# Optimization experiments

Hardware: AMD Instinct MI355X
Metric: run time of the kernel (lower is better)

Reference implementation:

```python
import jax, jax.numpy as jnp
import numpy as np

B, NB, H, E, NCT, NL = 16, 4096, 128, 65536, 32, 2
LN_EPS = 1e-5


def _layernorm(x, scale, bias):
    mu = jnp.mean(x, axis=-1, keepdims=True)
    var = jnp.var(x, axis=-1, keepdims=True)
    return (x - mu) / jnp.sqrt(var + LN_EPS) * scale + bias


def setup_inputs() -> dict:
    key = jax.random.key(0)
    ks = jax.random.split(key, 18)
    s = 1.0 / np.sqrt(H)
    inp = {
        'block_tokens': jax.random.normal(ks[0], (B, NB, H), jnp.float32),
        'edge_structure': jnp.full((E,), 0.5, jnp.float32),
        'ct_emb': 0.1 * jax.random.normal(ks[1], (NCT, E), jnp.float32),
        'W_proj': s * jax.random.normal(ks[2], (H, H), jnp.float32),
        'b_proj': jnp.zeros((H,), jnp.float32),
        'W_gate': (1.0 / np.sqrt(2 * H)) * jax.random.normal(ks[3], (2 * H, H), jnp.float32),
        'b_gate': jnp.zeros((H,), jnp.float32),
        'ln_scale': jnp.ones((NL, H), jnp.float32),
        'ln_bias': jnp.zeros((NL, H), jnp.float32),
        'W1': s * jax.random.normal(ks[4], (NL, H, 2 * H), jnp.float32),
        'b1': jnp.zeros((NL, 2 * H), jnp.float32),
        'W2': (1.0 / np.sqrt(2 * H)) * jax.random.normal(ks[5], (NL, 2 * H, H), jnp.float32),
        'b2': jnp.zeros((NL, H), jnp.float32),
        'cancer_type': jax.random.randint(ks[6], (B,), 0, NCT),
        'edge_src': jax.random.randint(ks[7], (E,), 0, NB),
        'edge_dst': jax.random.randint(ks[8], (E,), 0, NB),
        'block_active': jax.random.bernoulli(ks[9], 0.9, (B, NB)),
    }
    return inp


def reference(block_tokens, edge_structure, ct_emb, W_proj, b_proj, W_gate, b_gate,
              ln_scale, ln_bias, W1, b1, W2, b2,
              cancer_type, edge_src, edge_dst, block_active):
    # per-edge signed weights, masked by active src/dst blocks  -> (B, E)
    structure = jax.nn.sigmoid(edge_structure)
    edge_w = structure[None, :] * ct_emb[cancer_type]
    edge_w = edge_w * block_active[:, edge_src].astype(edge_w.dtype) \
                    * block_active[:, edge_dst].astype(edge_w.dtype)
    # route projection + ELU
    h_route = jax.nn.elu(jnp.einsum('bnh,hd->bnd', block_tokens, W_proj) + b_proj)
    # gather sources, weight, scatter-add to destinations
    weighted = edge_w[..., None] * h_route[:, edge_src, :]          # (B, E, H)
    messages = jnp.zeros_like(block_tokens).at[:, edge_dst, :].add(weighted)
    # gated residual
    gate = jax.nn.sigmoid(
        jnp.einsum('bnh,hd->bnd', jnp.concatenate([block_tokens, messages], axis=-1), W_gate) + b_gate)
    x = block_tokens + gate * messages
    # norm + FFN layers (dropout is identity at inference)
    for l in range(NL):
        normed = _layernorm(x, ln_scale[l], ln_bias[l])
        h = jax.nn.elu(jnp.einsum('bnh,hf->bnf', normed, W1[l]) + b1[l])
        x = x + jnp.einsum('bnf,fh->bnh', h, W2[l]) + b2[l]
    return (x, edge_w)
```

## Files before the change

kernel.cpp:

```cpp
#include <hip/hip_runtime.h>
#include <hip/hip_bf16.h>

#define BB     16
#define NBLK   4096
#define HD     128
#define NE     65536
#define MTOT   (BB * NBLK)

typedef __attribute__((ext_vector_type(8))) short bf16x8;
typedef __attribute__((ext_vector_type(4))) float f32x4;

__device__ __forceinline__ float bf2f(unsigned short u) {
    union { unsigned int i; float f; } v; v.i = ((unsigned int)u) << 16; return v.f;
}
__device__ __forceinline__ unsigned short f2bf(float f) {
    union { float f; unsigned int i; } v; v.f = f;
    unsigned int u = v.i;
    unsigned int r = u + 0x7FFFu + ((u >> 16) & 1u);
    return (unsigned short)(r >> 16);
}
__device__ __forceinline__ float ldf(const void* p, size_t i, int f32m) {
    return f32m ? ((const float*)p)[i] : bf2f(((const unsigned short*)p)[i]);
}
__device__ __forceinline__ int get_active(const void* p, int i, int mode) {
    switch (mode) {
        case 1:  return ((const unsigned char*)p)[i] != 0;
        case 2:  return ((const unsigned short*)p)[i] != 0;
        case 3:  return ((const float*)p)[i] != 0.f;
        default: return ((const int*)p)[i] != 0;
    }
}
__device__ __forceinline__ float elu_f(float v) {
    const float e = __expf(v);
    return v > 0.f ? v : e - 1.f;
}
__device__ __forceinline__ float sig_f(float v) {
    return 1.f / (1.f + __expf(-v));
}

__global__ void probe_k(const unsigned int* __restrict__ es,
                        const unsigned int* __restrict__ act,
                        int* __restrict__ flags)
{
    const int lane = threadIdx.x;
    const unsigned int v0 = act[lane], v1 = act[64 + lane];
    auto le1  = [](unsigned int v) { return v <= 1u; };
    auto byt  = [](unsigned int v) {
        return ((v & 0xFFu) <= 1u) && (((v >> 8) & 0xFFu) <= 1u) &&
               (((v >> 16) & 0xFFu) <= 1u) && ((v >> 24) <= 1u); };
    auto f32b = [](unsigned int v) { return v == 0u || v == 0x3F800000u; };
    auto bfb  = [](unsigned int v) {
        unsigned short h0 = (unsigned short)(v & 0xFFFFu), h1 = (unsigned short)(v >> 16);
        return (h0 == 0u || h0 == 0x3F80u) && (h1 == 0u || h1 == 0x3F80u); };
    const unsigned long long m_le1 = __ballot(le1(v0) && le1(v1));
    const unsigned long long m_byt = __ballot(byt(v0) && byt(v1));
    const unsigned long long m_f32 = __ballot(f32b(v0) && f32b(v1));
    const unsigned long long m_bf  = __ballot(bfb(v0) && bfb(v1));
    if (lane == 0) {
        flags[0] = (es[0] != 0x3F003F00u) ? 1 : 0;
        const unsigned long long full = ~0ull;
        flags[1] = (m_le1 == full) ? 0
                 : (m_byt == full) ? 1
                 : (m_f32 == full) ? 3
                 : (m_bf  == full) ? 2 : 0;
    }
}

__global__ __launch_bounds__(256) void cvt_k(const void* __restrict__ bt,
                                             unsigned short* __restrict__ bt16,
                                             const int* __restrict__ flags)
{
    const size_t i = ((size_t)blockIdx.x * 256 + threadIdx.x) * 8;
    if (flags[0]) {
        const float* q = (const float*)bt + i;
        f32x4 lo = *(const f32x4*)q;
        f32x4 hi = *(const f32x4*)(q + 4);
        bf16x8 r;
        #pragma unroll
        for (int j = 0; j < 4; ++j) { r[j] = (short)f2bf(lo[j]); r[4 + j] = (short)f2bf(hi[j]); }
        *(bf16x8*)(bt16 + i) = r;
    } else {
        *(bf16x8*)(bt16 + i) = *(const bf16x8*)((const unsigned short*)bt + i);
    }
}

__global__ __launch_bounds__(256) void transpose_k(
    const void* p0, const void* p1, const void* p2, const void* p3,
    const void* p4, const void* p5, unsigned short* __restrict__ wsT,
    const int* __restrict__ flags)
{
    const void* srcs[6]  = {p0, p1, p2, p3, p4, p5};
    const int eoffs[6]   = {0, 0, 0, 32768, 0, 32768};
    const int Ks[6]      = {128, 256, 128, 128, 256, 256};
    const int nsh[6]     = {7,   7,   8,   8,   7,   7};
    const int offs[6]    = {0, 16384, 49152, 81920, 114688, 147456};
    const int f32m = flags[0];
    const int z = blockIdx.y;
    const int K = Ks[z];
    const int Nn = 1 << nsh[z];
    const int idx = blockIdx.x * 256 + threadIdx.x;
    if (idx >= K * Nn) return;
    const int k = idx >> nsh[z];
    const int n = idx & (Nn - 1);
    wsT[offs[z] + n * K + k] = f2bf(ldf(srcs[z], (size_t)eoffs[z] + idx, f32m));
}

__global__ __launch_bounds__(256) void csr_count_k(const int* __restrict__ edst,
                                                   int* __restrict__ cnt)
{
    const int e = blockIdx.x * 256 + threadIdx.x;
    atomicAdd(&cnt[edst[e]], 1);
}

__global__ __launch_bounds__(1024) void csr_scan_k(const int* __restrict__ cnt,
                                                   int* __restrict__ ofs,
                                                   int* __restrict__ cur)
{
    __shared__ int part[1024];
    const int t = threadIdx.x;
    const int4 c = ((const int4*)cnt)[t];
    part[t] = c.x + c.y + c.z + c.w;
    __syncthreads();
    #pragma unroll
    for (int off = 1; off < 1024; off <<= 1) {
        const int v = (t >= off) ? part[t - off] : 0;
        __syncthreads();
        part[t] += v;
        __syncthreads();
    }
    const int base = t ? part[t - 1] : 0;
    int4 o;
    o.x = base; o.y = o.x + c.x; o.z = o.y + c.y; o.w = o.z + c.z;
    ((int4*)ofs)[t] = o;
    ((int4*)cur)[t] = o;
    if (t == 1023) ofs[4096] = part[1023];
}

__global__ __launch_bounds__(256) void csr_fill_k(const int* __restrict__ edst,
                                                  int* __restrict__ cur,
                                                  int* __restrict__ eidx,
                                                  int* __restrict__ pos_e)
{
    const int e = blockIdx.x * 256 + threadIdx.x;
    const int pos = atomicAdd(&cur[edst[e]], 1);
    eidx[pos] = e;
    pos_e[e] = pos;
}

__global__ __launch_bounds__(256) void edge_k(
    const void* __restrict__ es, const void* __restrict__ ctE,
    const int* __restrict__ ctype, const int* __restrict__ esrc, const int* __restrict__ edst,
    const void* __restrict__ act, const int* __restrict__ pos_e,
    float* __restrict__ out_ew, float2* __restrict__ compact,
    const int* __restrict__ flags)
{
    const int f32m = flags[0], am = flags[1];
    const int idx = blockIdx.x * 256 + threadIdx.x;
    const int b = idx >> 16;
    const int e = idx & 65535;
    const int s = esrc[e];
    const float sv  = sig_f(ldf(es, e, f32m));
    const float emb = ldf(ctE, (size_t)ctype[b] * NE + e, f32m);
    const int a1 = get_active(act, b * NBLK + s, am);
    const int a2 = get_active(act, b * NBLK + edst[e], am);
    const float w = (a1 && a2) ? sv * emb : 0.f;
    out_ew[idx] = w;
    compact[((size_t)b << 16) + pos_e[e]] = make_float2(w, __int_as_float(s));
}

__global__ __launch_bounds__(256) void gather_k(
    const float2* __restrict__ compact, const int* __restrict__ ofs,
    const unsigned short* __restrict__ hr, unsigned short* __restrict__ msg)
{
    const int blk = blockIdx.x;
    const int xcd = blk & 7;
    const int i   = blk >> 3;
    const int b   = xcd * 2 + (i & 1);
    const int d   = ((i >> 1) << 2) | (threadIdx.x >> 6);
    const int lane = threadIdx.x & 63;
    const int sub  = lane >> 4;
    const int l15  = lane & 15;
    const int j1 = ofs[d + 1];
    const size_t bbase = (size_t)b * NBLK * HD;
    const float2* cb = compact + ((size_t)b << 16);
    float acc[8];
    #pragma unroll
    for (int i2 = 0; i2 < 8; ++i2) acc[i2] = 0.f;
    int j = ofs[d] + sub;
    float2 c = (j < j1) ? cb[j] : make_float2(0.f, 0.f);
    while (j < j1) {
        const int jn = j + 4;
        const float2 cn = (jn < j1) ? cb[jn] : make_float2(0.f, 0.f);
        if (c.x != 0.f) {
            const int src = __float_as_int(c.y);
            const bf16x8 v = *(const bf16x8*)(hr + bbase + (size_t)src * HD + l15 * 8);
            #pragma unroll
            for (int i2 = 0; i2 < 8; ++i2)
                acc[i2] += c.x * bf2f((unsigned short)v[i2]);
        }
        c = cn; j = jn;
    }
    #pragma unroll
    for (int i2 = 0; i2 < 8; ++i2) {
        acc[i2] += __shfl_xor(acc[i2], 16);
        acc[i2] += __shfl_xor(acc[i2], 32);
    }
    if (sub == 0) {
        bf16x8 o;
        #pragma unroll
        for (int i2 = 0; i2 < 8; ++i2) o[i2] = (short)f2bf(acc[i2]);
        *(bf16x8*)(msg + bbase + (size_t)d * HD + l15 * 8) = o;
    }
}

template<int K, int N, int EPI>
__global__ __launch_bounds__(256) void gemm_k(
    const unsigned short* __restrict__ A,
    const unsigned short* __restrict__ WT,
    const void* __restrict__ bias, long boff,
    unsigned short* __restrict__ outb,
    const int* __restrict__ flags)
{
    constexpr int KI    = K / 32;
    constexpr int NCW   = N / 4;
    constexpr int NTW   = NCW / 16;
    constexpr int TILES = 8;
    constexpr int NBUF  = (K == 128 ? 4 : 2);
    const int f32m = flags[0];
    const int t    = threadIdx.x;
    const int lane = t & 63;
    const int wave = t >> 6;
    const int q    = lane >> 4;
    const int l15  = lane & 15;
    const int n0   = wave * NCW;

    bf16x8 Bf[KI][NTW];
    #pragma unroll
    for (int ki = 0; ki < KI; ++ki)
        #pragma unroll
        for (int nt = 0; nt < NTW; ++nt)
            Bf[ki][nt] = *(const bf16x8*)(WT + (size_t)(n0 + nt * 16 + l15) * K + ki * 32 + q * 8);

    float biasv[NTW];
    #pragma unroll
    for (int nt = 0; nt < NTW; ++nt)
        biasv[nt] = ldf(bias, boff + n0 + nt * 16 + l15, f32m);

    const int tile0 = blockIdx.x * TILES;
    bf16x8 Af[NBUF][KI];
    auto loadA = [&](int tt) {
        const int arow = (tile0 + tt) * 16 + l15;
        #pragma unroll
        for (int ki = 0; ki < KI; ++ki)
            Af[tt % NBUF][ki] = *(const bf16x8*)(A + (size_t)arow * K + ki * 32 + q * 8);
    };
    #pragma unroll
    for (int p = 0; p < NBUF; ++p) loadA(p);

    #pragma unroll
    for (int tt = 0; tt < TILES; ++tt) {
        const int s = tt % NBUF;
        f32x4 acc[NTW];
        #pragma unroll
        for (int i = 0; i < NTW; ++i) acc[i] = (f32x4){0.f, 0.f, 0.f, 0.f};
        #pragma unroll
        for (int ki = 0; ki < KI; ++ki)
            #pragma unroll
            for (int nt = 0; nt < NTW; ++nt)
                acc[nt] = __builtin_amdgcn_mfma_f32_16x16x32_bf16(Af[s][ki], Bf[ki][nt], acc[nt], 0, 0, 0);

        if (tt + NBUF < TILES) loadA(tt + NBUF);

        const int m0 = (tile0 + tt) * 16;
        #pragma unroll
        for (int nt = 0; nt < NTW; ++nt) {
            #pragma unroll
            for (int r = 0; r < 4; ++r) {
                const int row = m0 + q * 4 + r;
                const int col = n0 + nt * 16 + l15;
                const float v = acc[nt][r] + biasv[nt];
                outb[(size_t)row * N + col] = f2bf(elu_f(v));
            }
        }
    }
}

#define XI(tl, row, col)  x_lds[tl][row][((col) + 4 * (row)) & 127]
#define UIx(row, col)     U[row][((col) + 8 * (row)) & 255]

__global__ __launch_bounds__(256) void mega_k(
    const unsigned short* __restrict__ bt16,
    const unsigned short* __restrict__ msg,
    const void* __restrict__ btf,
    const unsigned short* __restrict__ WT,
    const void* __restrict__ bg,
    const void* __restrict__ b1, const void* __restrict__ b2,
    const void* __restrict__ lns, const void* __restrict__ lnb,
    float* __restrict__ xout,
    const int* __restrict__ flags)
{
    __shared__ __align__(16) float          x_lds[2][32][128];
    __shared__ __align__(16) unsigned short U[32][256];

    const int f32m = flags[0];
    const int t    = threadIdx.x;
    const int lane = t & 63;
    const int wave = t >> 6;
    const int q    = lane >> 4;
    const int l15  = lane & 15;
    const int base = blockIdx.x * 64;

    const int ng = wave * 32;
    const unsigned short* WgT = WT + 16384;

    bf16x8 Bg[8][2];
    #pragma unroll
    for (int ki = 0; ki < 8; ++ki)
        #pragma unroll
        for (int nt = 0; nt < 2; ++nt)
            Bg[ki][nt] = *(const bf16x8*)(WgT + (size_t)(ng + nt * 16 + l15) * 256 + ki * 32 + q * 8);
    float biasg[2];
    #pragma unroll
    for (int nt = 0; nt < 2; ++nt) biasg[nt] = ldf(bg, ng + nt * 16 + l15, f32m);

    #pragma unroll
    for (int tl = 0; tl < 2; ++tl) {
        const int row0 = base + tl * 32;
        bf16x8 Ag[2][8];
        #pragma unroll
        for (int tt = 0; tt < 2; ++tt) {
            const int arow = row0 + tt * 16 + l15;
            #pragma unroll
            for (int ki = 0; ki < 8; ++ki) {
                const int k = ki * 32 + q * 8;
                Ag[tt][ki] = (k < HD)
                    ? *(const bf16x8*)(bt16 + (size_t)arow * HD + k)
                    : *(const bf16x8*)(msg  + (size_t)arow * HD + (k - HD));
            }
        }
        float btv[2][2][4], mgv[2][2][4];
        #pragma unroll
        for (int tt = 0; tt < 2; ++tt)
            #pragma unroll
            for (int nt = 0; nt < 2; ++nt)
                #pragma unroll
                for (int r = 0; r < 4; ++r) {
                    const size_t gi = (size_t)(row0 + tt * 16 + q * 4 + r) * HD + ng + nt * 16 + l15;
                    btv[tt][nt][r] = ldf(btf, gi, f32m);
                    mgv[tt][nt][r] = bf2f(msg[gi]);
                }
        #pragma unroll
        for (int tt = 0; tt < 2; ++tt) {
            f32x4 acc[2];
            #pragma unroll
            for (int nt = 0; nt < 2; ++nt) acc[nt] = (f32x4){0.f, 0.f, 0.f, 0.f};
            __builtin_amdgcn_s_setprio(1);
            #pragma unroll
            for (int ki = 0; ki < 8; ++ki)
                #pragma unroll
                for (int nt = 0; nt < 2; ++nt)
                    acc[nt] = __builtin_amdgcn_mfma_f32_16x16x32_bf16(Ag[tt][ki], Bg[ki][nt], acc[nt], 0, 0, 0);
            __builtin_amdgcn_s_setprio(0);
            #pragma unroll
            for (int nt = 0; nt < 2; ++nt)
                #pragma unroll
                for (int r = 0; r < 4; ++r) {
                    const float g = sig_f(acc[nt][r] + biasg[nt]);
                    XI(tl, tt * 16 + q * 4 + r, ng + nt * 16 + l15) =
                        btv[tt][nt][r] + g * mgv[tt][nt][r];
                }
        }
    }
    __syncthreads();

    const int rowln = t >> 3;
    const int seg   = t & 7;
    const int n1 = wave * 64;
    const int n2 = wave * 32;

    #pragma unroll
    for (int l = 0; l < 2; ++l) {
        const unsigned short* W1T = WT + (l ? 81920  : 49152);
        const unsigned short* W2T = WT + (l ? 147456 : 114688);
        const long b1o = l ? 256 : 0, b2o = l ? 128 : 0, lno = l ? 128 : 0;

        bf16x8 B1[4][4];
        #pragma unroll
        for (int ki = 0; ki < 4; ++ki)
            #pragma unroll
            for (int nt = 0; nt < 4; ++nt)
                B1[ki][nt] = *(const bf16x8*)(W1T + (size_t)(n1 + nt * 16 + l15) * 128 + ki * 32 + q * 8);
        float bias1[4];
        #pragma unroll
        for (int nt = 0; nt < 4; ++nt) bias1[nt] = ldf(b1, b1o + n1 + nt * 16 + l15, f32m);
        bf16x8 B2[8][2];
        #pragma unroll
        for (int ki = 0; ki < 8; ++ki)
            #pragma unroll
            for (int nt = 0; nt < 2; ++nt)
                B2[ki][nt] = *(const bf16x8*)(W2T + (size_t)(n2 + nt * 16 + l15) * 256 + ki * 32 + q * 8);
        float bias2[2];
        #pragma unroll
        for (int nt = 0; nt < 2; ++nt) bias2[nt] = ldf(b2, b2o + n2 + nt * 16 + l15, f32m);

        float lsv[16], lbv[16];
        #pragma unroll
        for (int j = 0; j < 4; ++j)
            #pragma unroll
            for (int k = 0; k < 4; ++k) {
                const int col = seg * 16 + j * 4 + k;
                lsv[j * 4 + k] = ldf(lns, lno + col, f32m);
                lbv[j * 4 + k] = ldf(lnb, lno + col, f32m);
            }

        #pragma unroll
        for (int tl = 0; tl < 2; ++tl) {
            f32x4 xv[4];
            #pragma unroll
            for (int j = 0; j < 4; ++j)
                xv[j] = *(const f32x4*)&XI(tl, rowln, seg * 16 + j * 4);
            float s = 0.f, ss = 0.f;
            #pragma unroll
            for (int j = 0; j < 4; ++j)
                #pragma unroll
                for (int k = 0; k < 4; ++k) { const float v = xv[j][k]; s += v; ss += v * v; }
            #pragma unroll
            for (int off = 1; off < 8; off <<= 1) { s += __shfl_xor(s, off); ss += __shfl_xor(ss, off); }
            const float mu = s * (1.f / 128.f);
            const float rs = rsqrtf(ss * (1.f / 128.f) - mu * mu + 1e-5f);
            bf16x8 nv[2];
            #pragma unroll
            for (int j = 0; j < 4; ++j)
                #pragma unroll
                for (int k = 0; k < 4; ++k) {
                    const float nn = (xv[j][k] - mu) * rs * lsv[j * 4 + k] + lbv[j * 4 + k];
                    nv[j >> 1][(j & 1) * 4 + k] = (short)f2bf(nn);
                }
            *(bf16x8*)&UIx(rowln, seg * 16)     = nv[0];
            *(bf16x8*)&UIx(rowln, seg * 16 + 8) = nv[1];
            __syncthreads();

            bf16x8 An[2][4];
            #pragma unroll
            for (int tt = 0; tt < 2; ++tt)
                #pragma unroll
                for (int ki = 0; ki < 4; ++ki)
                    An[tt][ki] = *(const bf16x8*)&UIx(tt * 16 + l15, ki * 32 + q * 8);
            __syncthreads();

            #pragma unroll
            for (int tt = 0; tt < 2; ++tt) {
                f32x4 acc[4];
                #pragma unroll
                for (int nt = 0; nt < 4; ++nt) acc[nt] = (f32x4){0.f, 0.f, 0.f, 0.f};
                __builtin_amdgcn_s_setprio(1);
                #pragma unroll
                for (int ki = 0; ki < 4; ++ki)
                    #pragma unroll
                    for (int nt = 0; nt < 4; ++nt)
                        acc[nt] = __builtin_amdgcn_mfma_f32_16x16x32_bf16(An[tt][ki], B1[ki][nt], acc[nt], 0, 0, 0);
                __builtin_amdgcn_s_setprio(0);
                #pragma unroll
                for (int nt = 0; nt < 4; ++nt)
                    #pragma unroll
                    for (int r = 0; r < 4; ++r)
                        UIx(tt * 16 + q * 4 + r, n1 + nt * 16 + l15) =
                            f2bf(elu_f(acc[nt][r] + bias1[nt]));
            }
            __syncthreads();

            #pragma unroll
            for (int tt = 0; tt < 2; ++tt) {
                bf16x8 Ah[8];
                #pragma unroll
                for (int ki = 0; ki < 8; ++ki)
                    Ah[ki] = *(const bf16x8*)&UIx(tt * 16 + l15, ki * 32 + q * 8);
                f32x4 acc[2];
                #pragma unroll
                for (int nt = 0; nt < 2; ++nt) acc[nt] = (f32x4){0.f, 0.f, 0.f, 0.f};
                __builtin_amdgcn_s_setprio(1);
                #pragma unroll
                for (int ki = 0; ki < 8; ++ki)
                    #pragma unroll
                    for (int nt = 0; nt < 2; ++nt)
                        acc[nt] = __builtin_amdgcn_mfma_f32_16x16x32_bf16(Ah[ki], B2[ki][nt], acc[nt], 0, 0, 0);
                __builtin_amdgcn_s_setprio(0);
                #pragma unroll
                for (int nt = 0; nt < 2; ++nt)
                    #pragma unroll
                    for (int r = 0; r < 4; ++r)
                        XI(tl, tt * 16 + q * 4 + r, n2 + nt * 16 + l15) += acc[nt][r] + bias2[nt];
            }
            __syncthreads();
        }
    }

    #pragma unroll
    for (int tl = 0; tl < 2; ++tl) {
        float* xo = xout + (size_t)(base + tl * 32) * HD;
        #pragma unroll
        for (int j = 0; j < 4; ++j) {
            const int idx = j * 256 + t;
            const int r2  = idx >> 5;
            const int c4  = (idx & 31) * 4;
            *(f32x4*)(xo + (size_t)idx * 4) = *(const f32x4*)&XI(tl, r2, c4);
        }
    }
}

extern "C" void kernel_launch(void* const* d_in, const int* in_sizes, int n_in,
                              void* d_out, int out_size, void* d_ws, size_t ws_size,
                              hipStream_t stream)
{
    (void)in_sizes; (void)n_in; (void)out_size; (void)ws_size;

    const void* bt  = d_in[0];
    const void* es  = d_in[1];
    const void* ctE = d_in[2];
    const void* Wp  = d_in[3];
    const void* bp  = d_in[4];
    const void* Wg  = d_in[5];
    const void* bg  = d_in[6];
    const void* lns = d_in[7];
    const void* lnb = d_in[8];
    const void* W1  = d_in[9];
    const void* b1  = d_in[10];
    const void* W2  = d_in[11];
    const void* b2  = d_in[12];
    const int* ctype = (const int*)d_in[13];
    const int* esrc  = (const int*)d_in[14];
    const int* edst  = (const int*)d_in[15];
    const void* act  = d_in[16];

    float* out_x  = (float*)d_out;
    float* out_ew = out_x + (size_t)MTOT * HD;
    float* x = out_x;

    char* ws = (char*)d_ws;
    int*            flags = (int*)ws;
    unsigned short* msg   = (unsigned short*)(ws + 1024);
    unsigned short* bt16  = (unsigned short*)(ws + 1024 + (16ull << 20));
    unsigned short* hr    = (unsigned short*)(ws + 1024 + (32ull << 20));
    char* base48 = ws + 1024 + (48ull << 20);
    int*            cnt     = (int*)(base48);
    int*            ofs     = (int*)(base48 + (16 << 10));
    int*            cur     = (int*)(base48 + (36 << 10));
    int*            eidx    = (int*)(base48 + (52 << 10));
    int*            pos_e   = (int*)(base48 + (308 << 10));
    unsigned short* WT      = (unsigned short*)(base48 + (576 << 10));
    float2*         compact = (float2*)(base48 + (1 << 20));

    const int M = MTOT;

    probe_k<<<1, 64, 0, stream>>>((const unsigned int*)es, (const unsigned int*)act, flags);
    hipMemsetAsync(cnt, 0, NBLK * sizeof(int), stream);

    cvt_k<<<dim3((M * HD / 8) / 256), 256, 0, stream>>>(bt, bt16, flags);
    transpose_k<<<dim3(128, 6), 256, 0, stream>>>(Wp, Wg, W1, W1, W2, W2, WT, flags);

    csr_count_k<<<dim3(NE / 256), 256, 0, stream>>>(edst, cnt);
    csr_scan_k<<<dim3(1), 1024, 0, stream>>>(cnt, ofs, cur);
    csr_fill_k<<<dim3(NE / 256), 256, 0, stream>>>(edst, cur, eidx, pos_e);

    edge_k<<<dim3((BB * NE) / 256), 256, 0, stream>>>(
        es, ctE, ctype, esrc, edst, act, pos_e, out_ew, compact, flags);

    gemm_k<128, 128, 0><<<dim3(M / 128), 256, 0, stream>>>(
        bt16, WT + 0, bp, 0, hr, flags);

    gather_k<<<dim3(M / 4), 256, 0, stream>>>(compact, ofs, hr, msg);

    mega_k<<<dim3(M / 64), 256, 0, stream>>>(
        bt16, msg, bt, WT, bg, b1, b2, lns, lnb, x, flags);
}
```

Baseline: 315.8 us.

## Double mega_k block to 512 threads, batch tiles per barrier, cut register pressure

The fused gate/LN/FFN kernel now runs 512 threads per block, with two halves of four waves each handling 64 rows, so each block covers 128 rows and the grid is halved. Syncthreads are batched across both 32-row tiles per layer, which cuts the number of barriers. W2 fragments are loaded later and the layernorm scale/bias are read inline instead of held in registers, which lowers register pressure so the 512,2 launch bound can fit. LDS use roughly doubles, and the larger barriers involve more waves, so occupancy and stall behaviour shift.

```diff
diff --git a/kernel.cpp b/kernel.cpp
--- a/kernel.cpp
+++ b/kernel.cpp
@@ -285,10 +285,10 @@
     }
 }
 
-#define XI(tl, row, col)  x_lds[tl][row][((col) + 4 * (row)) & 127]
-#define UIx(row, col)     U[row][((col) + 8 * (row)) & 255]
-
-__global__ __launch_bounds__(256) void mega_k(
+#define XI(xt, row, col)      x_lds[xt][row][((col) + 4 * (row)) & 127]
+#define UI(hf, tl, row, col)  U[hf][tl][row][((col) + 8 * (row)) & 255]
+
+__global__ __launch_bounds__(512, 2) void mega_k(
     const unsigned short* __restrict__ bt16,
     const unsigned short* __restrict__ msg,
     const void* __restrict__ btf,
@@ -299,18 +299,20 @@
     float* __restrict__ xout,
     const int* __restrict__ flags)
 {
-    __shared__ __align__(16) float          x_lds[2][32][128];
-    __shared__ __align__(16) unsigned short U[32][256];
+    __shared__ __align__(16) float          x_lds[4][32][128];
+    __shared__ __align__(16) unsigned short U[2][2][32][256];
 
     const int f32m = flags[0];
     const int t    = threadIdx.x;
     const int lane = t & 63;
     const int wave = t >> 6;
+    const int hf   = wave >> 2;
+    const int wv   = wave & 3;
     const int q    = lane >> 4;
     const int l15  = lane & 15;
-    const int base = blockIdx.x * 64;
-
-    const int ng = wave * 32;
+    const int rhf  = blockIdx.x * 128 + hf * 64;
+
+    const int ng = wv * 32;
     const unsigned short* WgT = WT + 16384;
 
     bf16x8 Bg[8][2];
@@ -325,32 +327,27 @@
 
     #pragma unroll
     for (int tl = 0; tl < 2; ++tl) {
-        const int row0 = base + tl * 32;
-        bf16x8 Ag[2][8];
+        const int xt = hf * 2 + tl;
         #pragma unroll
         for (int tt = 0; tt < 2; ++tt) {
-            const int arow = row0 + tt * 16 + l15;
+            const int arow = rhf + tl * 32 + tt * 16;
+            bf16x8 Ag[8];
             #pragma unroll
             for (int ki = 0; ki < 8; ++ki) {
                 const int k = ki * 32 + q * 8;
-                Ag[tt][ki] = (k < HD)
-                    ? *(const bf16x8*)(bt16 + (size_t)arow * HD + k)
-                    : *(const bf16x8*)(msg  + (size_t)arow * HD + (k - HD));
+                Ag[ki] = (k < HD)
+                    ? *(const bf16x8*)(bt16 + (size_t)(arow + l15) * HD + k)
+                    : *(const bf16x8*)(msg  + (size_t)(arow + l15) * HD + (k - HD));
             }
-        }
-        float btv[2][2][4], mgv[2][2][4];
-        #pragma unroll
-        for (int tt = 0; tt < 2; ++tt)
+            float btv[2][4], mgv[2][4];
             #pragma unroll
             for (int nt = 0; nt < 2; ++nt)
                 #pragma unroll
                 for (int r = 0; r < 4; ++r) {
-                    const size_t gi = (size_t)(row0 + tt * 16 + q * 4 + r) * HD + ng + nt * 16 + l15;
-                    btv[tt][nt][r] = ldf(btf, gi, f32m);
-                    mgv[tt][nt][r] = bf2f(msg[gi]);
+                    const size_t gi = (size_t)(arow + q * 4 + r) * HD + ng + nt * 16 + l15;
+                    btv[nt][r] = ldf(btf, gi, f32m);
+                    mgv[nt][r] = bf2f(msg[gi]);
                 }
-        #pragma unroll
-        for (int tt = 0; tt < 2; ++tt) {
             f32x4 acc[2];
             #pragma unroll
             for (int nt = 0; nt < 2; ++nt) acc[nt] = (f32x4){0.f, 0.f, 0.f, 0.f};
@@ -359,24 +356,24 @@
             for (int ki = 0; ki < 8; ++ki)
                 #pragma unroll
                 for (int nt = 0; nt < 2; ++nt)
-                    acc[nt] = __builtin_amdgcn_mfma_f32_16x16x32_bf16(Ag[tt][ki], Bg[ki][nt], acc[nt], 0, 0, 0);
+                    acc[nt] = __builtin_amdgcn_mfma_f32_16x16x32_bf16(Ag[ki], Bg[ki][nt], acc[nt], 0, 0, 0);
             __builtin_amdgcn_s_setprio(0);
             #pragma unroll
             for (int nt = 0; nt < 2; ++nt)
                 #pragma unroll
                 for (int r = 0; r < 4; ++r) {
                     const float g = sig_f(acc[nt][r] + biasg[nt]);
-                    XI(tl, tt * 16 + q * 4 + r, ng + nt * 16 + l15) =
-                        btv[tt][nt][r] + g * mgv[tt][nt][r];
+                    XI(xt, tt * 16 + q * 4 + r, ng + nt * 16 + l15) =
+                        btv[nt][r] + g * mgv[nt][r];
                 }
         }
     }
     __syncthreads();
 
-    const int rowln = t >> 3;
+    const int rowln = (t & 255) >> 3;
     const int seg   = t & 7;
-    const int n1 = wave * 64;
-    const int n2 = wave * 32;
+    const int n1 = wv * 64;
+    const int n2 = wv * 32;
 
     #pragma unroll
     for (int l = 0; l < 2; ++l) {
@@ -393,32 +390,14 @@
         float bias1[4];
         #pragma unroll
         for (int nt = 0; nt < 4; ++nt) bias1[nt] = ldf(b1, b1o + n1 + nt * 16 + l15, f32m);
-        bf16x8 B2[8][2];
-        #pragma unroll
-        for (int ki = 0; ki < 8; ++ki)
-            #pragma unroll
-            for (int nt = 0; nt < 2; ++nt)
-                B2[ki][nt] = *(const bf16x8*)(W2T + (size_t)(n2 + nt * 16 + l15) * 256 + ki * 32 + q * 8);
-        float bias2[2];
-        #pragma unroll
-        for (int nt = 0; nt < 2; ++nt) bias2[nt] = ldf(b2, b2o + n2 + nt * 16 + l15, f32m);
-
-        float lsv[16], lbv[16];
-        #pragma unroll
-        for (int j = 0; j < 4; ++j)
-            #pragma unroll
-            for (int k = 0; k < 4; ++k) {
-                const int col = seg * 16 + j * 4 + k;
-                lsv[j * 4 + k] = ldf(lns, lno + col, f32m);
-                lbv[j * 4 + k] = ldf(lnb, lno + col, f32m);
-            }
 
         #pragma unroll
         for (int tl = 0; tl < 2; ++tl) {
+            const int xt = hf * 2 + tl;
             f32x4 xv[4];
             #pragma unroll
             for (int j = 0; j < 4; ++j)
-                xv[j] = *(const f32x4*)&XI(tl, rowln, seg * 16 + j * 4);
+                xv[j] = *(const f32x4*)&XI(xt, rowln, seg * 16 + j * 4);
             float s = 0.f, ss = 0.f;
             #pragma unroll
             for (int j = 0; j < 4; ++j)
@@ -433,21 +412,28 @@
             for (int j = 0; j < 4; ++j)
                 #pragma unroll
                 for (int k = 0; k < 4; ++k) {
-                    const float nn = (xv[j][k] - mu) * rs * lsv[j * 4 + k] + lbv[j * 4 + k];
+                    const int col = seg * 16 + j * 4 + k;
+                    const float nn = (xv[j][k] - mu) * rs * ldf(lns, lno + col, f32m)
+                                     + ldf(lnb, lno + col, f32m);
                     nv[j >> 1][(j & 1) * 4 + k] = (short)f2bf(nn);
                 }
-            *(bf16x8*)&UIx(rowln, seg * 16)     = nv[0];
-            *(bf16x8*)&UIx(rowln, seg * 16 + 8) = nv[1];
-            __syncthreads();
-
-            bf16x8 An[2][4];
+            *(bf16x8*)&UI(hf, tl, rowln, seg * 16)     = nv[0];
+            *(bf16x8*)&UI(hf, tl, rowln, seg * 16 + 8) = nv[1];
+        }
+        __syncthreads();
+
+        bf16x8 An[2][2][4];
+        #pragma unroll
+        for (int tl = 0; tl < 2; ++tl)
             #pragma unroll
             for (int tt = 0; tt < 2; ++tt)
                 #pragma unroll
                 for (int ki = 0; ki < 4; ++ki)
-                    An[tt][ki] = *(const bf16x8*)&UIx(tt * 16 + l15, ki * 32 + q * 8);
-            __syncthreads();
-
+                    An[tl][tt][ki] = *(const bf16x8*)&UI(hf, tl, tt * 16 + l15, ki * 32 + q * 8);
+        __syncthreads();
+
+        #pragma unroll
+        for (int tl = 0; tl < 2; ++tl)
             #pragma unroll
             for (int tt = 0; tt < 2; ++tt) {
                 f32x4 acc[4];
@@ -458,23 +444,36 @@
                 for (int ki = 0; ki < 4; ++ki)
                     #pragma unroll
                     for (int nt = 0; nt < 4; ++nt)
-                        acc[nt] = __builtin_amdgcn_mfma_f32_16x16x32_bf16(An[tt][ki], B1[ki][nt], acc[nt], 0, 0, 0);
+                        acc[nt] = __builtin_amdgcn_mfma_f32_16x16x32_bf16(An[tl][tt][ki], B1[ki][nt], acc[nt], 0, 0, 0);
                 __builtin_amdgcn_s_setprio(0);
                 #pragma unroll
                 for (int nt = 0; nt < 4; ++nt)
                     #pragma unroll
                     for (int r = 0; r < 4; ++r)
-                        UIx(tt * 16 + q * 4 + r, n1 + nt * 16 + l15) =
+                        UI(hf, tl, tt * 16 + q * 4 + r, n1 + nt * 16 + l15) =
                             f2bf(elu_f(acc[nt][r] + bias1[nt]));
             }
-            __syncthreads();
-
+
+        bf16x8 B2[8][2];
+        #pragma unroll
+        for (int ki = 0; ki < 8; ++ki)
+            #pragma unroll
+            for (int nt = 0; nt < 2; ++nt)
+                B2[ki][nt] = *(const bf16x8*)(W2T + (size_t)(n2 + nt * 16 + l15) * 256 + ki * 32 + q * 8);
+        float bias2[2];
+        #pragma unroll
+        for (int nt = 0; nt < 2; ++nt) bias2[nt] = ldf(b2, b2o + n2 + nt * 16 + l15, f32m);
+        __syncthreads();
+
+        #pragma unroll
+        for (int tl = 0; tl < 2; ++tl) {
+            const int xt = hf * 2 + tl;
             #pragma unroll
             for (int tt = 0; tt < 2; ++tt) {
                 bf16x8 Ah[8];
                 #pragma unroll
                 for (int ki = 0; ki < 8; ++ki)
-                    Ah[ki] = *(const bf16x8*)&UIx(tt * 16 + l15, ki * 32 + q * 8);
+                    Ah[ki] = *(const bf16x8*)&UI(hf, tl, tt * 16 + l15, ki * 32 + q * 8);
                 f32x4 acc[2];
                 #pragma unroll
                 for (int nt = 0; nt < 2; ++nt) acc[nt] = (f32x4){0.f, 0.f, 0.f, 0.f};
@@ -489,21 +488,21 @@
                 for (int nt = 0; nt < 2; ++nt)
                     #pragma unroll
                     for (int r = 0; r < 4; ++r)
-                        XI(tl, tt * 16 + q * 4 + r, n2 + nt * 16 + l15) += acc[nt][r] + bias2[nt];
+                        XI(xt, tt * 16 + q * 4 + r, n2 + nt * 16 + l15) += acc[nt][r] + bias2[nt];
             }
-            __syncthreads();
         }
-    }
-
-    #pragma unroll
-    for (int tl = 0; tl < 2; ++tl) {
-        float* xo = xout + (size_t)(base + tl * 32) * HD;
-        #pragma unroll
-        for (int j = 0; j < 4; ++j) {
-            const int idx = j * 256 + t;
+        __syncthreads();
+    }
+
+    #pragma unroll
+    for (int xt = 0; xt < 4; ++xt) {
+        float* xo = xout + (size_t)(blockIdx.x * 128 + xt * 32) * HD;
+        #pragma unroll
+        for (int j = 0; j < 2; ++j) {
+            const int idx = j * 512 + t;
             const int r2  = idx >> 5;
             const int c4  = (idx & 31) * 4;
-            *(f32x4*)(xo + (size_t)idx * 4) = *(const f32x4*)&XI(tl, r2, c4);
+            *(f32x4*)(xo + (size_t)idx * 4) = *(const f32x4*)&XI(xt, r2, c4);
         }
     }
 }
@@ -570,6 +569,6 @@
 
     gather_k<<<dim3(M / 4), 256, 0, stream>>>(compact, ofs, hr, msg);
 
-    mega_k<<<dim3(M / 64), 256, 0, stream>>>(
+    mega_k<<<dim3(M / 128), 512, 0, stream>>>(
         bt16, msg, bt, WT, bg, b1, b2, lns, lnb, x, flags);
 }
```

Result: faster. 300.9 us (-4.7%).
